# Performance work log

Hardware: AMD Instinct MI355X
Metric: run time of the kernel (lower is better)

The kernel has to match this reference:

```python
import jax, jax.numpy as jnp
import numpy as np


def setup_inputs() -> dict:
    key = jax.random.key(0)
    k1, k2, k3, k4 = jax.random.split(key, 4)
    B, L1, L2, H, A = 64, 512, 512, 1024, 1024
    reps_lt = jax.random.normal(k1, (B, L1, H), dtype=jnp.float32)
    reps_rt = jax.random.normal(k2, (B, L2, H), dtype=jnp.float32)
    mask_lt = jnp.ones((B, L1), dtype=jnp.float32)
    mask_rt = jnp.ones((B, L2), dtype=jnp.float32)
    # Keras 'uniform' initializer ~ U(-0.05, 0.05); scale similarly
    attn_w1 = jax.random.uniform(k3, (H, A), dtype=jnp.float32, minval=-0.05, maxval=0.05)
    diagonal_W = jax.random.uniform(k4, (1, 1, A), dtype=jnp.float32, minval=-0.05, maxval=0.05)
    return {
        "reps_lt": reps_lt,
        "reps_rt": reps_rt,
        "mask_lt": mask_lt,
        "mask_rt": mask_rt,
        "attn_w1": attn_w1,
        "diagonal_W": diagonal_W,
    }


def reference(reps_lt, reps_rt, mask_lt, mask_rt, attn_w1, diagonal_W):
    # Projections: the original does expand_dims + broadcast multiply + sum,
    # which is mathematically a matmul over the hidden dim.
    # attn_w2 aliases attn_w1 because hidden dims are equal.
    attn_lt = jnp.tanh(jnp.einsum('blh,ha->bla', reps_lt, attn_w1))  # [B,L1,A]
    attn_rt = jnp.tanh(jnp.einsum('brh,ha->bra', reps_rt, attn_w1))  # [B,L2,A]
    attn_lt = attn_lt * diagonal_W                                   # diagonal bilinear scale
    # batch_dot([B,L1,A], [B,A,L2]) -> [B,L1,L2]
    attn_value = jnp.einsum('bla,bra->blr', attn_lt, attn_rt)
    # mask (multiplicative, as in original) before softmax
    attn_value = attn_value * mask_lt[:, :, None] * mask_rt[:, None, :]
    attn_prob = jax.nn.softmax(attn_value, axis=-1)
    # mask again after softmax
    attn_prob = attn_prob * mask_lt[:, :, None] * mask_rt[:, None, :]
    return attn_prob
```

## Files before the change

### kernel.cpp

```cpp
#include <hip/hip_runtime.h>
#include <hip/hip_bf16.h>

#define B_ 64
#define L_ 512
#define H_ 1024
#define A_ 1024

typedef short bf16x8 __attribute__((ext_vector_type(8)));
typedef float f32x4 __attribute__((ext_vector_type(4)));

__device__ __forceinline__ void gld16(const void* g, void* l) {
  __builtin_amdgcn_global_load_lds((const __attribute__((address_space(1))) void*)g,
                                   (__attribute__((address_space(3))) void*)l, 16, 0, 0);
}

__device__ __forceinline__ unsigned short f2bf(float f) {
  unsigned u = __builtin_bit_cast(unsigned, f);
  u = (u + 0x7fffu + ((u >> 16) & 1u)) >> 16;
  return (unsigned short)u;
}

__device__ __forceinline__ unsigned short cvtbf(float f) {
  __hip_bfloat16 b = __float2bfloat16(f);
  return __builtin_bit_cast(unsigned short, b);
}

__device__ __forceinline__ float fast_tanh(float x) {
  float e = __expf(2.f * x);
  float r = __builtin_amdgcn_rcpf(e + 1.f);
  return __builtin_fmaf(-2.f, r, 1.f);
}

__global__ __launch_bounds__(256) void cvt_kernel(const float* __restrict__ lt,
                                                  const float* __restrict__ rt,
                                                  unsigned short* __restrict__ xb) {
  const size_t NC = (size_t)B_ * L_ * H_ / 8;
  size_t stride = (size_t)gridDim.x * blockDim.x;
  for (size_t c = (size_t)blockIdx.x * blockDim.x + threadIdx.x; c < 2 * NC; c += stride) {
    const float* src = (c < NC) ? (lt + c * 8) : (rt + (c - NC) * 8);
    float4 v0 = ((const float4*)src)[0];
    float4 v1 = ((const float4*)src)[1];
    bf16x8 o;
    o[0] = (short)cvtbf(v0.x); o[1] = (short)cvtbf(v0.y);
    o[2] = (short)cvtbf(v0.z); o[3] = (short)cvtbf(v0.w);
    o[4] = (short)cvtbf(v1.x); o[5] = (short)cvtbf(v1.y);
    o[6] = (short)cvtbf(v1.z); o[7] = (short)cvtbf(v1.w);
    *(bf16x8*)(xb + c * 8) = o;
  }
}

__global__ __launch_bounds__(256) void wtrans_kernel(const float* __restrict__ W,
                                                     unsigned short* __restrict__ Wt) {
  __shared__ float tile[32][33];
  int tx = threadIdx.x & 31, ty = threadIdx.x >> 5;
  int a0 = (blockIdx.x & 31) << 5, h0 = (blockIdx.x >> 5) << 5;
#pragma unroll
  for (int i = 0; i < 4; ++i) {
    int h = ty + i * 8;
    tile[h][tx] = W[(size_t)(h0 + h) * A_ + a0 + tx];
  }
  __syncthreads();
#pragma unroll
  for (int i = 0; i < 4; ++i) {
    int a = ty + i * 8;
    Wt[(size_t)(a0 + a) * H_ + h0 + tx] = f2bf(tile[tx][a]);
  }
}

#define STG_FROM(gptr, Ls, buf, h, kt_) {                                  \
    const unsigned short* g_ = (gptr) + (size_t)(h) * 128 * H_ + (kt_) * 64; \
    gld16(g_, &Ls[buf][(h) * 8192 + lofs]);                                \
    gld16(g_ + (size_t)64 * H_, &Ls[buf][(h) * 8192 + 4096 + lofs]); }

#define LOAD_BQ(Bsrc, buf) { _Pragma("unroll") for (int ni = 0; ni < 4; ++ni) { \
    int brow = wc * 64 + ni * 16 + l15;                                    \
    bq[ni][0] = *(const bf16x8*)&Bsrc[buf][brow * 64 + rd0];               \
    bq[ni][1] = *(const bf16x8*)&Bsrc[buf][brow * 64 + rd1]; } }

#define PHASE(Asrc, q, buf, STAGE_OP, CKPT) {                              \
    bf16x8 aq0, aq1, aq2, aq3;                                             \
    { int ar = wr * 128 + (q) * 32 + l15;                                  \
      aq0 = *(const bf16x8*)&Asrc[buf][ar * 64 + rd0];                     \
      aq1 = *(const bf16x8*)&Asrc[buf][ar * 64 + rd1];                     \
      aq2 = *(const bf16x8*)&Asrc[buf][(ar + 16) * 64 + rd0];              \
      aq3 = *(const bf16x8*)&Asrc[buf][(ar + 16) * 64 + rd1]; }            \
    STAGE_OP;                                                              \
    asm volatile("s_barrier" ::: "memory");                                \
    __builtin_amdgcn_s_setprio(1);                                         \
    _Pragma("unroll") for (int ni = 0; ni < 4; ++ni) {                     \
      acc[(q)*2][ni] = __builtin_amdgcn_mfma_f32_16x16x32_bf16(            \
          aq0, bq[ni][0], acc[(q)*2][ni], 0, 0, 0);                        \
      acc[(q)*2][ni] = __builtin_amdgcn_mfma_f32_16x16x32_bf16(            \
          aq1, bq[ni][1], acc[(q)*2][ni], 0, 0, 0);                        \
      acc[(q)*2+1][ni] = __builtin_amdgcn_mfma_f32_16x16x32_bf16(          \
          aq2, bq[ni][0], acc[(q)*2+1][ni], 0, 0, 0);                      \
      acc[(q)*2+1][ni] = __builtin_amdgcn_mfma_f32_16x16x32_bf16(          \
          aq3, bq[ni][1], acc[(q)*2+1][ni], 0, 0, 0); }                    \
    __builtin_amdgcn_s_setprio(0);                                         \
    if (CKPT) asm volatile("s_waitcnt vmcnt(4)" ::: "memory");             \
    asm volatile("s_barrier" ::: "memory"); }

#define CONVEYOR(gA_, gB_)                                                 \
  STG_FROM(gB_, Bs, 0, 0, 0); STG_FROM(gB_, Bs, 0, 1, 0);                  \
  STG_FROM(gA_, As, 0, 0, 0); STG_FROM(gA_, As, 0, 1, 0);                  \
  STG_FROM(gB_, Bs, 1, 0, 1); STG_FROM(gB_, Bs, 1, 1, 1);                  \
  asm volatile("s_waitcnt vmcnt(4)" ::: "memory");                         \
  asm volatile("s_barrier" ::: "memory");                                  \
  for (int i = 0; i < 8; ++i) {                                            \
    int kt1 = 2 * i + 1;                                                   \
    int kt2 = (2 * i + 2) & 15, kt3 = (2 * i + 3) & 15;                    \
    LOAD_BQ(Bs, 0);                                                        \
    PHASE(As, 0, 0, STG_FROM(gA_, As, 1, 0, kt1), 0);                      \
    PHASE(As, 1, 0, STG_FROM(gA_, As, 1, 1, kt1), 0);                      \
    PHASE(As, 2, 0, STG_FROM(gB_, Bs, 0, 0, kt2), 0);                      \
    PHASE(As, 3, 0, STG_FROM(gB_, Bs, 0, 1, kt2), 1);                      \
    LOAD_BQ(Bs, 1);                                                        \
    PHASE(As, 0, 1, STG_FROM(gA_, As, 0, 0, kt2), 0);                      \
    PHASE(As, 1, 1, STG_FROM(gA_, As, 0, 1, kt2), 0);                      \
    PHASE(As, 2, 1, STG_FROM(gB_, Bs, 1, 0, kt3), 0);                      \
    PHASE(As, 3, 1, STG_FROM(gB_, Bs, 1, 1, kt3), 1);                      \
  }

__global__ __launch_bounds__(512, 2) void proj8_kernel(
    const unsigned short* __restrict__ Xb, const unsigned short* __restrict__ Wt,
    const float* __restrict__ diag, unsigned short* __restrict__ Pb) {
  __shared__ unsigned short As[2][256 * 64];
  __shared__ unsigned short Bs[2][256 * 64];
  int t = threadIdx.x;
  int lane = t & 63, wave = t >> 6;
  int wr = wave >> 2, wc = wave & 3;
  int l15 = lane & 15, l4 = lane >> 4;

  int bid = (int)blockIdx.x;
  int x = bid & 7, k = bid >> 3;
  int mt = x + 8 * (k >> 2);
  int nt = k & 3;
  int mrow0 = mt << 8, ncol0 = nt << 8;
  int isLt = (mt < 128);

  int rs = t >> 3, ss = t & 7;
  const unsigned short* gA = Xb + (size_t)(mrow0 + rs) * H_ + ((ss ^ (rs & 7)) << 3);
  const unsigned short* gB = Wt + (size_t)(ncol0 + rs) * H_ + ((ss ^ (rs & 7)) << 3);
  int lofs = (rs * 8 + ss) * 8;

  int rd0 = (l4 ^ (l15 & 7)) * 8;
  int rd1 = ((4 + l4) ^ (l15 & 7)) * 8;

  f32x4 acc[8][4] = {};
  bf16x8 bq[4][2];

  CONVEYOR(gA, gB);

#pragma unroll
  for (int mi = 0; mi < 8; ++mi) {
#pragma unroll
    for (int ni = 0; ni < 4; ++ni) {
      int col = ncol0 + wc * 64 + ni * 16 + l15;
      float d = isLt ? diag[col] : 1.0f;
#pragma unroll
      for (int rr = 0; rr < 4; ++rr) {
        int row = mrow0 + wr * 128 + mi * 16 + l4 * 4 + rr;
        Pb[(size_t)row * A_ + col] = f2bf(fast_tanh(acc[mi][ni][rr]) * d);
      }
    }
  }
}

__global__ __launch_bounds__(512, 2) void score8_kernel(
    const unsigned short* __restrict__ Pb,
    const float* __restrict__ mask_lt, const float* __restrict__ mask_rt,
    float* __restrict__ out) {
  __shared__ unsigned short As[2][256 * 64];
  __shared__ unsigned short Bs[2][256 * 64];
  int t = threadIdx.x;
  int lane = t & 63, wave = t >> 6;
  int wr = wave >> 2, wc = wave & 3;
  int l15 = lane & 15, l4 = lane >> 4;

  int bid = (int)blockIdx.x;
  int x = bid & 7, k = bid >> 3;
  int pm = x + 8 * (k >> 1);
  int b = pm >> 1, mt = pm & 1, nt = k & 1;

  int arow0 = b * 512 + mt * 256;
  int brow0 = 32768 + b * 512 + nt * 256;

  int rs = t >> 3, ss = t & 7;
  const unsigned short* gA = Pb + (size_t)(arow0 + rs) * H_ + ((ss ^ (rs & 7)) << 3);
  const unsigned short* gB = Pb + (size_t)(brow0 + rs) * H_ + ((ss ^ (rs & 7)) << 3);
  int lofs = (rs * 8 + ss) * 8;

  int rd0 = (l4 ^ (l15 & 7)) * 8;
  int rd1 = ((4 + l4) ^ (l15 & 7)) * 8;

  f32x4 acc[8][4] = {};
  bf16x8 bq[4][2];

  CONVEYOR(gA, gB);

  const float* mlp = mask_lt + b * L_;
  const float* mrp = mask_rt + b * L_;
  float* obase = out + (size_t)b * L_ * L_;
#pragma unroll
  for (int mi = 0; mi < 8; ++mi) {
#pragma unroll
    for (int ni = 0; ni < 4; ++ni) {
      int col = nt * 256 + wc * 64 + ni * 16 + l15;
      float mr = mrp[col];
#pragma unroll
      for (int rr = 0; rr < 4; ++rr) {
        int row = mt * 256 + wr * 128 + mi * 16 + l4 * 4 + rr;
        obase[(size_t)row * L_ + col] = acc[mi][ni][rr] * mlp[row] * mr;
      }
    }
  }
}

__global__ __launch_bounds__(256) void softmax_kernel(float* __restrict__ out,
                                                      const float* __restrict__ mask_lt,
                                                      const float* __restrict__ mask_rt) {
  int lane = threadIdx.x & 63, wave = threadIdx.x >> 6;
  int row = (int)blockIdx.x * 4 + wave;
  int b = row >> 9;
  float* p = out + (size_t)row * L_;
  float4 v0 = *(const float4*)(p + lane * 8);
  float4 v1 = *(const float4*)(p + lane * 8 + 4);
  float m = fmaxf(fmaxf(fmaxf(v0.x, v0.y), fmaxf(v0.z, v0.w)),
                  fmaxf(fmaxf(v1.x, v1.y), fmaxf(v1.z, v1.w)));
#pragma unroll
  for (int off = 32; off; off >>= 1) m = fmaxf(m, __shfl_xor(m, off));
  float e0 = __expf(v0.x - m), e1 = __expf(v0.y - m), e2 = __expf(v0.z - m), e3 = __expf(v0.w - m);
  float e4 = __expf(v1.x - m), e5 = __expf(v1.y - m), e6 = __expf(v1.z - m), e7 = __expf(v1.w - m);
  float s = ((e0 + e1) + (e2 + e3)) + ((e4 + e5) + (e6 + e7));
#pragma unroll
  for (int off = 32; off; off >>= 1) s += __shfl_xor(s, off);
  float sc = (1.0f / s) * mask_lt[row];
  const float* mrp = mask_rt + (b << 9) + lane * 8;
  float4 mr0 = *(const float4*)mrp;
  float4 mr1 = *(const float4*)(mrp + 4);
  float4 o0 = make_float4(e0 * sc * mr0.x, e1 * sc * mr0.y, e2 * sc * mr0.z, e3 * sc * mr0.w);
  float4 o1 = make_float4(e4 * sc * mr1.x, e5 * sc * mr1.y, e6 * sc * mr1.z, e7 * sc * mr1.w);
  *(float4*)(p + lane * 8) = o0;
  *(float4*)(p + lane * 8 + 4) = o1;
}

extern "C" void kernel_launch(void* const* d_in, const int* in_sizes, int n_in,
                              void* d_out, int out_size, void* d_ws, size_t ws_size,
                              hipStream_t stream) {
  const float* reps_lt = (const float*)d_in[0];
  const float* reps_rt = (const float*)d_in[1];
  const float* mask_lt = (const float*)d_in[2];
  const float* mask_rt = (const float*)d_in[3];
  const float* attn_w1 = (const float*)d_in[4];
  const float* diag    = (const float*)d_in[5];
  float* out = (float*)d_out;

  unsigned short* wt  = (unsigned short*)d_ws;
  unsigned short* pb  = wt + (size_t)H_ * A_;
  unsigned short* xb  = pb + (size_t)B_ * L_ * A_ * 2;

  hipLaunchKernelGGL(wtrans_kernel, dim3(1024), dim3(256), 0, stream, attn_w1, wt);
  hipLaunchKernelGGL(cvt_kernel, dim3(8192), dim3(256), 0, stream,
                     reps_lt, reps_rt, xb);
  hipLaunchKernelGGL(proj8_kernel, dim3(1024), dim3(512), 0, stream,
                     xb, wt, diag, pb);
  hipLaunchKernelGGL(score8_kernel, dim3(256), dim3(512), 0, stream,
                     pb, mask_lt, mask_rt, out);
  hipLaunchKernelGGL(softmax_kernel, dim3(8192), dim3(256), 0, stream,
                     out, mask_lt, mask_rt);
}
```

Baseline: 299.3 us.

## Fuse fp32-to-bf16 input conversion into projection GEMM loads

Removes the separate conversion kernel that wrote bf16 copies of both input activation tensors. The projection kernel now streams fp32 activations straight into LDS through a triple-buffered pipeline and converts them to bf16 while loading MFMA fragments. This avoids one full write and re-read of the activations in HBM. In exchange, each tile moves twice the bytes per element into LDS, the kernel does extra conversion ALU work inside the main loop, and the K-step shrinks to 32, which adds more barriers.

After: 312.1 us. 4.3% more time.

```diff
diff --git a/kernel.cpp b/kernel.cpp
--- a/kernel.cpp
+++ b/kernel.cpp
@@ -29,24 +29,6 @@
   float e = __expf(2.f * x);
   float r = __builtin_amdgcn_rcpf(e + 1.f);
   return __builtin_fmaf(-2.f, r, 1.f);
-}
-
-__global__ __launch_bounds__(256) void cvt_kernel(const float* __restrict__ lt,
-                                                  const float* __restrict__ rt,
-                                                  unsigned short* __restrict__ xb) {
-  const size_t NC = (size_t)B_ * L_ * H_ / 8;
-  size_t stride = (size_t)gridDim.x * blockDim.x;
-  for (size_t c = (size_t)blockIdx.x * blockDim.x + threadIdx.x; c < 2 * NC; c += stride) {
-    const float* src = (c < NC) ? (lt + c * 8) : (rt + (c - NC) * 8);
-    float4 v0 = ((const float4*)src)[0];
-    float4 v1 = ((const float4*)src)[1];
-    bf16x8 o;
-    o[0] = (short)cvtbf(v0.x); o[1] = (short)cvtbf(v0.y);
-    o[2] = (short)cvtbf(v0.z); o[3] = (short)cvtbf(v0.w);
-    o[4] = (short)cvtbf(v1.x); o[5] = (short)cvtbf(v1.y);
-    o[6] = (short)cvtbf(v1.z); o[7] = (short)cvtbf(v1.w);
-    *(bf16x8*)(xb + c * 8) = o;
-  }
 }
 
 __global__ __launch_bounds__(256) void wtrans_kernel(const float* __restrict__ W,
@@ -64,6 +46,145 @@
   for (int i = 0; i < 4; ++i) {
     int a = ty + i * 8;
     Wt[(size_t)(a0 + a) * H_ + h0 + tx] = f2bf(tile[tx][a]);
+  }
+}
+
+__global__ __launch_bounds__(512, 2) void projf_kernel(
+    const float* __restrict__ Xlt, const float* __restrict__ Xrt,
+    const unsigned short* __restrict__ Wt, const float* __restrict__ diag,
+    unsigned short* __restrict__ Pb) {
+  __shared__ float Af[3][256 * 32];
+  __shared__ unsigned short Bb[3][256 * 32];
+  int t = threadIdx.x;
+  int lane = t & 63, wave = t >> 6;
+  int wr = wave >> 2, wc = wave & 3;
+  int l15 = lane & 15, l4 = lane >> 4;
+
+  int bid = (int)blockIdx.x;
+  int x = bid & 7, k = bid >> 3;
+  int mt = x + 8 * (k >> 2);
+  int nt = k & 3;
+  int mrow0 = mt << 8, ncol0 = nt << 8;
+  int isLt = (mt < 128);
+  const float* X = isLt ? Xlt : Xrt;
+  int xrow0 = (isLt ? mt : mt - 128) << 8;
+
+  const float* gAsrc[4];
+  int adst[4];
+#pragma unroll
+  for (int u = 0; u < 4; ++u) {
+    int ci = u * 512 + t;
+    int r = ci >> 3, c = ci & 7;
+    gAsrc[u] = X + (size_t)(xrow0 + r) * H_ + ((c ^ (r & 7)) << 2);
+    adst[u] = ci * 4;
+  }
+  const unsigned short* gBsrc[2];
+  int bdst[2];
+#pragma unroll
+  for (int u = 0; u < 2; ++u) {
+    int ci = u * 512 + t;
+    int r = ci >> 2, c = ci & 3;
+    gBsrc[u] = Wt + (size_t)(ncol0 + r) * H_ + ((c ^ ((r >> 1) & 3)) << 3);
+    bdst[u] = ci * 8;
+  }
+
+#define STGA(buf, kt_) {                                   \
+    gld16(gAsrc[0] + (kt_) * 32, &Af[buf][adst[0]]);       \
+    gld16(gAsrc[1] + (kt_) * 32, &Af[buf][adst[1]]);       \
+    gld16(gAsrc[2] + (kt_) * 32, &Af[buf][adst[2]]);       \
+    gld16(gAsrc[3] + (kt_) * 32, &Af[buf][adst[3]]); }
+#define STGB(buf, kt_) {                                   \
+    gld16(gBsrc[0] + (kt_) * 32, &Bb[buf][bdst[0]]);       \
+    gld16(gBsrc[1] + (kt_) * 32, &Bb[buf][bdst[1]]); }
+
+  int s0 = ((2 * l4) ^ (l15 & 7)) * 4;
+  int rdB = (l4 ^ ((l15 >> 1) & 3)) * 8;
+
+  f32x4 acc[8][4] = {};
+
+  STGA(0, 0); STGB(0, 0);
+  STGA(1, 1); STGB(1, 1);
+  asm volatile("s_waitcnt vmcnt(6)" ::: "memory");
+  asm volatile("s_barrier" ::: "memory");
+
+  int cur = 0;
+  for (int kt = 0; kt < 32; ++kt) {
+    int nxt = cur + 2; if (nxt >= 3) nxt -= 3;
+    bool st = (kt <= 29);
+    const float* Ac = Af[cur];
+    const unsigned short* Bc = Bb[cur];
+
+    bf16x8 bq[4];
+#pragma unroll
+    for (int ni = 0; ni < 4; ++ni)
+      bq[ni] = *(const bf16x8*)&Bc[(wc * 64 + ni * 16 + l15) * 32 + rdB];
+    bf16x8 aq[4];
+#pragma unroll
+    for (int f = 0; f < 4; ++f) {
+      const float* base = &Ac[(wr * 128 + f * 16 + l15) * 32];
+      float4 v0 = *(const float4*)(base + s0);
+      float4 v1 = *(const float4*)(base + (s0 ^ 4));
+      bf16x8 a;
+      a[0] = (short)cvtbf(v0.x); a[1] = (short)cvtbf(v0.y);
+      a[2] = (short)cvtbf(v0.z); a[3] = (short)cvtbf(v0.w);
+      a[4] = (short)cvtbf(v1.x); a[5] = (short)cvtbf(v1.y);
+      a[6] = (short)cvtbf(v1.z); a[7] = (short)cvtbf(v1.w);
+      aq[f] = a;
+    }
+    if (st) STGA(nxt, kt + 2);
+    asm volatile("s_barrier" ::: "memory");
+    __builtin_amdgcn_s_setprio(1);
+#pragma unroll
+    for (int f = 0; f < 4; ++f)
+#pragma unroll
+      for (int ni = 0; ni < 4; ++ni)
+        acc[f][ni] = __builtin_amdgcn_mfma_f32_16x16x32_bf16(aq[f], bq[ni], acc[f][ni], 0, 0, 0);
+    __builtin_amdgcn_s_setprio(0);
+    asm volatile("s_barrier" ::: "memory");
+
+#pragma unroll
+    for (int f = 0; f < 4; ++f) {
+      const float* base = &Ac[(wr * 128 + 64 + f * 16 + l15) * 32];
+      float4 v0 = *(const float4*)(base + s0);
+      float4 v1 = *(const float4*)(base + (s0 ^ 4));
+      bf16x8 a;
+      a[0] = (short)cvtbf(v0.x); a[1] = (short)cvtbf(v0.y);
+      a[2] = (short)cvtbf(v0.z); a[3] = (short)cvtbf(v0.w);
+      a[4] = (short)cvtbf(v1.x); a[5] = (short)cvtbf(v1.y);
+      a[6] = (short)cvtbf(v1.z); a[7] = (short)cvtbf(v1.w);
+      aq[f] = a;
+    }
+    if (st) STGB(nxt, kt + 2);
+    asm volatile("s_barrier" ::: "memory");
+    __builtin_amdgcn_s_setprio(1);
+#pragma unroll
+    for (int f = 0; f < 4; ++f)
+#pragma unroll
+      for (int ni = 0; ni < 4; ++ni)
+        acc[4 + f][ni] = __builtin_amdgcn_mfma_f32_16x16x32_bf16(aq[f], bq[ni], acc[4 + f][ni], 0, 0, 0);
+    __builtin_amdgcn_s_setprio(0);
+    if (kt < 30)
+      asm volatile("s_waitcnt vmcnt(6)" ::: "memory");
+    else
+      asm volatile("s_waitcnt vmcnt(0)" ::: "memory");
+    asm volatile("s_barrier" ::: "memory");
+    cur = (cur == 2) ? 0 : cur + 1;
+  }
+#undef STGA
+#undef STGB
+
+#pragma unroll
+  for (int mi = 0; mi < 8; ++mi) {
+#pragma unroll
+    for (int ni = 0; ni < 4; ++ni) {
+      int col = ncol0 + wc * 64 + ni * 16 + l15;
+      float d = isLt ? diag[col] : 1.0f;
+#pragma unroll
+      for (int rr = 0; rr < 4; ++rr) {
+        int row = mrow0 + wr * 128 + mi * 16 + l4 * 4 + rr;
+        Pb[(size_t)row * A_ + col] = f2bf(fast_tanh(acc[mi][ni][rr]) * d);
+      }
+    }
   }
 }
 
@@ -121,51 +242,6 @@
     PHASE(As, 3, 1, STG_FROM(gB_, Bs, 1, 1, kt3), 1);                      \
   }
 
-__global__ __launch_bounds__(512, 2) void proj8_kernel(
-    const unsigned short* __restrict__ Xb, const unsigned short* __restrict__ Wt,
-    const float* __restrict__ diag, unsigned short* __restrict__ Pb) {
-  __shared__ unsigned short As[2][256 * 64];
-  __shared__ unsigned short Bs[2][256 * 64];
-  int t = threadIdx.x;
-  int lane = t & 63, wave = t >> 6;
-  int wr = wave >> 2, wc = wave & 3;
-  int l15 = lane & 15, l4 = lane >> 4;
-
-  int bid = (int)blockIdx.x;
-  int x = bid & 7, k = bid >> 3;
-  int mt = x + 8 * (k >> 2);
-  int nt = k & 3;
-  int mrow0 = mt << 8, ncol0 = nt << 8;
-  int isLt = (mt < 128);
-
-  int rs = t >> 3, ss = t & 7;
-  const unsigned short* gA = Xb + (size_t)(mrow0 + rs) * H_ + ((ss ^ (rs & 7)) << 3);
-  const unsigned short* gB = Wt + (size_t)(ncol0 + rs) * H_ + ((ss ^ (rs & 7)) << 3);
-  int lofs = (rs * 8 + ss) * 8;
-
-  int rd0 = (l4 ^ (l15 & 7)) * 8;
-  int rd1 = ((4 + l4) ^ (l15 & 7)) * 8;
-
-  f32x4 acc[8][4] = {};
-  bf16x8 bq[4][2];
-
-  CONVEYOR(gA, gB);
-
-#pragma unroll
-  for (int mi = 0; mi < 8; ++mi) {
-#pragma unroll
-    for (int ni = 0; ni < 4; ++ni) {
-      int col = ncol0 + wc * 64 + ni * 16 + l15;
-      float d = isLt ? diag[col] : 1.0f;
-#pragma unroll
-      for (int rr = 0; rr < 4; ++rr) {
-        int row = mrow0 + wr * 128 + mi * 16 + l4 * 4 + rr;
-        Pb[(size_t)row * A_ + col] = f2bf(fast_tanh(acc[mi][ni][rr]) * d);
-      }
-    }
-  }
-}
-
 __global__ __launch_bounds__(512, 2) void score8_kernel(
     const unsigned short* __restrict__ Pb,
     const float* __restrict__ mask_lt, const float* __restrict__ mask_rt,
@@ -255,15 +331,12 @@
   const float* diag    = (const float*)d_in[5];
   float* out = (float*)d_out;
 
-  unsigned short* wt  = (unsigned short*)d_ws;
-  unsigned short* pb  = wt + (size_t)H_ * A_;
-  unsigned short* xb  = pb + (size_t)B_ * L_ * A_ * 2;
+  unsigned short* wt = (unsigned short*)d_ws;
+  unsigned short* pb = wt + (size_t)H_ * A_;
 
   hipLaunchKernelGGL(wtrans_kernel, dim3(1024), dim3(256), 0, stream, attn_w1, wt);
-  hipLaunchKernelGGL(cvt_kernel, dim3(8192), dim3(256), 0, stream,
-                     reps_lt, reps_rt, xb);
-  hipLaunchKernelGGL(proj8_kernel, dim3(1024), dim3(512), 0, stream,
-                     xb, wt, diag, pb);
+  hipLaunchKernelGGL(projf_kernel, dim3(1024), dim3(512), 0, stream,
+                     reps_lt, reps_rt, wt, diag, pb);
   hipLaunchKernelGGL(score8_kernel, dim3(256), dim3(512), 0, stream,
                      pb, mask_lt, mask_rt, out);
   hipLaunchKernelGGL(softmax_kernel, dim3(8192), dim3(256), 0, stream,
```
